# Kernel tuning notes

Measured on AMD Instinct MI355X. Metric: run time of the kernel, lower is better.

## Reference

```python
import jax, jax.numpy as jnp
import numpy as np

N_NODES = 100000
N_EDGES = 1600000
D = 64
NUM_HOPS = 3


def setup_inputs() -> dict:
    key = jax.random.key(0)
    ks = jax.random.split(key, 8)
    return {
        "H_l": jax.random.normal(ks[0], (N_NODES, D), dtype=jnp.float32),
        "edge_row": jax.random.randint(ks[1], (N_EDGES,), 0, N_NODES, dtype=jnp.int64),
        "edge_col": jax.random.randint(ks[2], (N_EDGES,), 0, N_NODES, dtype=jnp.int64),
        "edge_val": jax.random.uniform(ks[3], (N_EDGES,), dtype=jnp.float32),
        "out_degree": jax.random.uniform(ks[4], (N_NODES,), dtype=jnp.float32),
        "in_degree": jax.random.uniform(ks[5], (N_NODES,), dtype=jnp.float32),
        "hop_attention": jnp.ones((NUM_HOPS,), dtype=jnp.float32),
        "theta_out": jnp.full((NUM_HOPS,), 0.5, dtype=jnp.float32),
        "theta_in": jnp.full((NUM_HOPS,), 0.5, dtype=jnp.float32),
        "Theta": jax.random.normal(ks[6], (D, D), dtype=jnp.float32) * (6.0 ** 0.5) / (2 * D) ** 0.5,
    }


def reference(H_l, edge_row, edge_col, edge_val, out_degree, in_degree,
              hop_attention, theta_out, theta_in, Theta):
    n = H_l.shape[0]
    num_hops = hop_attention.shape[0]
    alpha = jax.nn.softmax(hop_attention)

    def spmm(rows, cols, X):
        # (A @ X)[r] = sum over edges (r,c): val * X[c]
        return jax.ops.segment_sum(edge_val[:, None] * X[cols], rows, num_segments=n)

    # fixed degree-scaled features (degrees clamped as in __init__)
    X_out = jnp.maximum(out_degree, 1e-8)[:, None] * H_l
    X_in = jnp.maximum(in_degree, 1e-8)[:, None] * H_l
    sum_term = jnp.zeros_like(H_l)
    for k in range(num_hops):
        # A^{k+1} @ (D_out H) computed by one more application of A per hop
        X_out = spmm(edge_row, edge_col, X_out)
        # (A^{k+1})^T @ (D_in H): transpose swaps row/col roles
        X_in = spmm(edge_col, edge_row, X_in)
        sum_term = sum_term + alpha[k] * (theta_out[k] * X_out + theta_in[k] * X_in)

    conv_term = jax.nn.sigmoid(sum_term @ Theta)
    return conv_term + H_l
```

## Files before the change

### kernel.cpp

```cpp
#include <hip/hip_runtime.h>
#include <hip/hip_fp16.h>

#define DFEAT 64
#define BKT_SHIFT 8
#define BKT_NODES 256
#define NBMAX 512
#define CH 4096
#define SRC_BITS 18
#define SRC_MASK ((1 << SRC_BITS) - 1)

__device__ __forceinline__ unsigned short f2h(float f) {
    return __half_as_ushort(__float2half(f));
}
__device__ __forceinline__ float h2f(unsigned short u) {
    return __half2float(__ushort_as_half(u));
}

__global__ void init_kernel(const float* __restrict__ H,
                            const float* __restrict__ outdeg,
                            const float* __restrict__ indeg,
                            const float* __restrict__ hop_att,
                            const float* __restrict__ th_out,
                            const float* __restrict__ th_in,
                            unsigned short* __restrict__ XAout,
                            unsigned short* __restrict__ XAin,
                            float* __restrict__ coefs, int n4) {
    int idx = blockIdx.x * blockDim.x + threadIdx.x;
    if (idx == 0) {
        float m = fmaxf(fmaxf(hop_att[0], hop_att[1]), hop_att[2]);
        float e0 = __expf(hop_att[0] - m);
        float e1 = __expf(hop_att[1] - m);
        float e2 = __expf(hop_att[2] - m);
        float inv = 1.0f / (e0 + e1 + e2);
        coefs[0] = e0 * inv * th_out[0]; coefs[1] = e0 * inv * th_in[0];
        coefs[2] = e1 * inv * th_out[1]; coefs[3] = e1 * inv * th_in[1];
        coefs[4] = e2 * inv * th_out[2]; coefs[5] = e2 * inv * th_in[2];
    }
    if (idx >= n4) return;
    int row = idx >> 4;
    float4 h = reinterpret_cast<const float4*>(H)[idx];
    float doo = fmaxf(outdeg[row], 1e-8f);
    float dii = fmaxf(indeg[row], 1e-8f);
    reinterpret_cast<ushort4*>(XAout)[idx] =
        make_ushort4(f2h(h.x * doo), f2h(h.y * doo), f2h(h.z * doo), f2h(h.w * doo));
    reinterpret_cast<ushort4*>(XAin)[idx] =
        make_ushort4(f2h(h.x * dii), f2h(h.y * dii), f2h(h.z * dii), f2h(h.w * dii));
}

__global__ __launch_bounds__(256) void hist2d_kernel(
        const int* __restrict__ erow, const int* __restrict__ ecol,
        int* __restrict__ cnt2, int nEdges, int nB, int nBlkA) {
    __shared__ int hR[NBMAX], hC[NBMAX];
    int k = blockIdx.x;
    for (int i = threadIdx.x; i < nB; i += 256) { hR[i] = 0; hC[i] = 0; }
    __syncthreads();
    int base = k * CH;
    int nV = min(CH, nEdges - base);
    for (int i = threadIdx.x; i < nV; i += 256) {
        atomicAdd(&hR[erow[base + i] >> BKT_SHIFT], 1);
        atomicAdd(&hC[ecol[base + i] >> BKT_SHIFT], 1);
    }
    __syncthreads();
    for (int b = threadIdx.x; b < nB; b += 256) {
        cnt2[(size_t)b * nBlkA + k] = hR[b];
        cnt2[((size_t)nB + b) * nBlkA + k] = hC[b];
    }
}

__global__ void scan_reduce1(const int* __restrict__ p, int* __restrict__ bsum,
                             int n) {
    int t = threadIdx.x, lane = t & 63, wid = t >> 6;
    int base = blockIdx.x * 1024 + t * 4;
    int s = 0;
#pragma unroll
    for (int i = 0; i < 4; ++i) { int idx = base + i; if (idx < n) s += p[idx]; }
#pragma unroll
    for (int o = 32; o >= 1; o >>= 1) s += __shfl_down(s, o, 64);
    __shared__ int wsum[4];
    if (lane == 0) wsum[wid] = s;
    __syncthreads();
    if (t == 0) bsum[blockIdx.x] = wsum[0] + wsum[1] + wsum[2] + wsum[3];
}

__global__ void scan_spine1(int* __restrict__ bsum, int nChunks) {
    int lane = threadIdx.x;
    int carry = 0;
    for (int base = 0; base < nChunks; base += 64) {
        int i = base + lane;
        int v = (i < nChunks) ? bsum[i] : 0;
        int s = v;
#pragma unroll
        for (int o = 1; o < 64; o <<= 1) {
            int x = __shfl_up(s, o, 64);
            if (lane >= o) s += x;
        }
        if (i < nChunks) bsum[i] = carry + s - v;
        carry += __shfl(s, 63, 64);
    }
}

__global__ void scan_down1(int* __restrict__ p, const int* __restrict__ bsum,
                           int n) {
    int t = threadIdx.x, lane = t & 63, wid = t >> 6;
    int base = blockIdx.x * 1024 + t * 4;
    int v[4];
    int tsum = 0;
#pragma unroll
    for (int i = 0; i < 4; ++i) {
        v[i] = (base + i < n) ? p[base + i] : 0;
        tsum += v[i];
    }
    int inc = tsum;
#pragma unroll
    for (int o = 1; o < 64; o <<= 1) {
        int x = __shfl_up(inc, o, 64);
        if (lane >= o) inc += x;
    }
    __shared__ int wsum[4];
    if (lane == 63) wsum[wid] = inc;
    __syncthreads();
    int woff = 0;
    for (int w = 0; w < wid; ++w) woff += wsum[w];
    int run = bsum[blockIdx.x] + woff + inc - tsum;
#pragma unroll
    for (int i = 0; i < 4; ++i) {
        if (base + i < n) p[base + i] = run;
        run += v[i];
    }
}

__global__ __launch_bounds__(256) void partA_kernel(
        const int* __restrict__ erow, const int* __restrict__ ecol,
        const float* __restrict__ eval, const int* __restrict__ base2,
        int2* __restrict__ recR, int2* __restrict__ recC,
        int nEdges, int nB, int nBlkA) {
    __shared__ int hist[NBMAX], scn[NBMAX], cur[NBMAX], gbase[NBMAX];
    __shared__ unsigned short keybuf[CH], slotKey[CH];
    __shared__ int2 stage[CH];
    int dir = blockIdx.y;
    const int* dk = dir ? ecol : erow;
    const int* ds = dir ? erow : ecol;
    int2* rec = dir ? recC : recR;
    int k = blockIdx.x;
    int base = k * CH;
    int nV = min(CH, nEdges - base);
    for (int i = threadIdx.x; i < nB; i += 256) {
        hist[i] = 0; cur[i] = 0;
        gbase[i] = base2[((size_t)dir * nB + i) * nBlkA + k] - dir * nEdges;
    }
    __syncthreads();
    for (int i = threadIdx.x; i < nV; i += 256) {
        int key = dk[base + i] >> BKT_SHIFT;
        keybuf[i] = (unsigned short)key;
        atomicAdd(&hist[key], 1);
    }
    __syncthreads();
    if (threadIdx.x < 64) {
        int lane = threadIdx.x;
        int carry = 0;
        for (int bb = 0; bb < nB; bb += 64) {
            int i = bb + lane;
            int v = (i < nB) ? hist[i] : 0;
            int s = v;
#pragma unroll
            for (int o = 1; o < 64; o <<= 1) {
                int x = __shfl_up(s, o, 64);
                if (lane >= o) s += x;
            }
            if (i < nB) scn[i] = carry + s - v;
            carry += __shfl(s, 63, 64);
        }
    }
    __syncthreads();
    for (int i = threadIdx.x; i < nV; i += 256) {
        int e = base + i;
        int key = keybuf[i];
        int slot = scn[key] + atomicAdd(&cur[key], 1);
        int dl = dk[e] & (BKT_NODES - 1);
        stage[slot] = make_int2(ds[e] | (dl << SRC_BITS), __float_as_int(eval[e]));
        slotKey[slot] = (unsigned short)key;
    }
    __syncthreads();
    for (int i = threadIdx.x; i < nV; i += 256) {
        int key = slotKey[i];
        rec[gbase[key] + (i - scn[key])] = stage[i];
    }
}

__global__ __launch_bounds__(256) void partB_kernel(
        const int2* __restrict__ recR, const int2* __restrict__ recC,
        const int* __restrict__ base2,
        int* __restrict__ rowptr, int* __restrict__ colptr,
        unsigned* __restrict__ pairsR, unsigned* __restrict__ pairsC,
        int nEdges, int nB, int nBlkA, int nNodes) {
    __shared__ int hist[BKT_NODES], scn[BKT_NODES], cur[BKT_NODES];
    int dir = blockIdx.y;
    int b = blockIdx.x;
    const int2* rec = dir ? recC : recR;
    unsigned* pairs = dir ? pairsC : pairsR;
    int* nptr = dir ? colptr : rowptr;
    int segB = base2[((size_t)dir * nB + b) * nBlkA] - dir * nEdges;
    int segE = (b == nB - 1) ? nEdges
             : base2[((size_t)dir * nB + b + 1) * nBlkA] - dir * nEdges;
    int t = threadIdx.x;
    hist[t] = 0; cur[t] = 0;
    __syncthreads();
    for (int j = segB + t; j < segE; j += 256)
        atomicAdd(&hist[(rec[j].x >> SRC_BITS) & (BKT_NODES - 1)], 1);
    __syncthreads();
    if (t < 64) {
        int lane = t, carry = 0;
        for (int bb = 0; bb < BKT_NODES; bb += 64) {
            int i = bb + lane;
            int v = hist[i], s = v;
#pragma unroll
            for (int o = 1; o < 64; o <<= 1) {
                int x = __shfl_up(s, o, 64);
                if (lane >= o) s += x;
            }
            scn[i] = carry + s - v;
            carry += __shfl(s, 63, 64);
        }
    }
    __syncthreads();
    int node = (b << BKT_SHIFT) + t;
    if (node < nNodes) nptr[node] = segB + scn[t];
    if (b == nB - 1 && t == 0) nptr[nNodes] = nEdges;
    for (int j = segB + t; j < segE; j += 256) {
        int2 r = rec[j];
        int dl = (r.x >> SRC_BITS) & (BKT_NODES - 1);
        int slot = segB + scn[dl] + atomicAdd(&cur[dl], 1);
        unsigned vh = f2h(__int_as_float(r.y)) & 0x7FFFu;
        pairs[slot] = ((unsigned)(r.x & SRC_MASK) << 15) | vh;
    }
}

template <int FIRST, int LAST>
__global__ __launch_bounds__(256) void spmm_split(
        const int* __restrict__ rowptr, const unsigned* __restrict__ pairsR,
        const int* __restrict__ colptr, const unsigned* __restrict__ pairsC,
        const __half* __restrict__ Xout, const __half* __restrict__ Xin,
        unsigned short* __restrict__ Yout, unsigned short* __restrict__ Yin,
        unsigned short* __restrict__ sumO, unsigned short* __restrict__ sumI,
        const float* __restrict__ coefs, int k, int nNodes) {
    int b = blockIdx.x;
    int slot = b & 7;
    int dir = slot >> 2;
    int g = (b >> 3) * 4 + (slot & 3);
    int wid = threadIdx.x >> 6;
    int lane = threadIdx.x & 63;
    int node = g * 4 + wid;
    if (node >= nNodes) return;

    const int* ptr = dir ? colptr : rowptr;
    const unsigned* pairs = dir ? pairsC : pairsR;
    const __half* X = dir ? Xin : Xout;
    unsigned short* Y = dir ? Yin : Yout;
    unsigned short* sm = dir ? sumI : sumO;
    float cf = coefs[2 * k + dir];

    int hb = lane >> 5;
    int sub = lane & 31;

    float2 a0 = {0.f, 0.f}, a1 = {0.f, 0.f}, a2 = {0.f, 0.f}, a3 = {0.f, 0.f};
    int bE = ptr[node], eE = ptr[node + 1];
    int j = bE;
    for (; j + 8 <= eE; j += 8) {
        unsigned p0 = pairs[j     + hb];
        unsigned p1 = pairs[j + 2 + hb];
        unsigned p2 = pairs[j + 4 + hb];
        unsigned p3 = pairs[j + 6 + hb];
        float2 x0 = __half22float2(*(const __half2*)(X + (p0 >> 15) * DFEAT + 2 * sub));
        float2 x1 = __half22float2(*(const __half2*)(X + (p1 >> 15) * DFEAT + 2 * sub));
        float2 x2 = __half22float2(*(const __half2*)(X + (p2 >> 15) * DFEAT + 2 * sub));
        float2 x3 = __half22float2(*(const __half2*)(X + (p3 >> 15) * DFEAT + 2 * sub));
        float v0 = h2f(p0 & 0x7FFFu);
        float v1 = h2f(p1 & 0x7FFFu);
        float v2 = h2f(p2 & 0x7FFFu);
        float v3 = h2f(p3 & 0x7FFFu);
        a0.x += v0 * x0.x; a0.y += v0 * x0.y;
        a1.x += v1 * x1.x; a1.y += v1 * x1.y;
        a2.x += v2 * x2.x; a2.y += v2 * x2.y;
        a3.x += v3 * x3.x; a3.y += v3 * x3.y;
    }
    if (j < eE) {
#pragma unroll
        for (int q = 0; q < 4; ++q) {
            int idx = j + 2 * q + hb;
            unsigned p = (idx < eE) ? pairs[idx] : 0u;
            float2 x = __half22float2(*(const __half2*)(X + (p >> 15) * DFEAT + 2 * sub));
            float v = h2f(p & 0x7FFFu);
            a0.x += v * x.x; a0.y += v * x.y;
        }
    }
    float ax = (a0.x + a1.x) + (a2.x + a3.x);
    float ay = (a0.y + a1.y) + (a2.y + a3.y);
    ax += __shfl_xor(ax, 32, 64);
    ay += __shfl_xor(ay, 32, 64);

    if (hb == 0) {
        int off = node * DFEAT + 2 * sub;
        if (!LAST) {
            __half2 yv = __floats2half2_rn(ax, ay);
            __builtin_nontemporal_store(*reinterpret_cast<unsigned*>(&yv),
                                        reinterpret_cast<unsigned*>(Y + off));
        }
        float sx = cf * ax, sy = cf * ay;
        if (!FIRST) {
            __half2 old = *reinterpret_cast<const __half2*>(sm + off);
            float2 of = __half22float2(old);
            sx += of.x; sy += of.y;
        }
        __half2 sv = __floats2half2_rn(sx, sy);
        __builtin_nontemporal_store(*reinterpret_cast<unsigned*>(&sv),
                                    reinterpret_cast<unsigned*>(sm + off));
    }
}

__global__ __launch_bounds__(256) void final_kernel(
        const unsigned short* __restrict__ sumO,
        const unsigned short* __restrict__ sumI,
        const float* __restrict__ H, const float* __restrict__ Theta,
        float* __restrict__ out, int nRows) {
    __shared__ float Th[64 * 64];
    __shared__ float Srow[4 * 64];
    int t = threadIdx.x;
    for (int i = t; i < 64 * 64; i += 256) Th[i] = Theta[i];
    int rl = t >> 6;
    int c = t & 63;
    int row = blockIdx.x * 4 + rl;
    int off = row * DFEAT + c;
    float sv = (row < nRows) ? h2f(sumO[off]) + h2f(sumI[off]) : 0.f;
    Srow[rl * 64 + c] = sv;
    __syncthreads();
    if (row >= nRows) return;
    float acc = 0.f;
#pragma unroll
    for (int kk = 0; kk < 64; ++kk) acc += Srow[rl * 64 + kk] * Th[kk * 64 + c];
    float r = 1.0f / (1.0f + __expf(-acc)) + H[off];
    __builtin_nontemporal_store(r, &out[off]);
}

extern "C" void kernel_launch(void* const* d_in, const int* in_sizes, int n_in,
                              void* d_out, int out_size, void* d_ws, size_t ws_size,
                              hipStream_t stream) {
    const float* H      = (const float*)d_in[0];
    const int*   erow   = (const int*)d_in[1];
    const int*   ecol   = (const int*)d_in[2];
    const float* eval   = (const float*)d_in[3];
    const float* outdeg = (const float*)d_in[4];
    const float* indeg  = (const float*)d_in[5];
    const float* hopatt = (const float*)d_in[6];
    const float* thout  = (const float*)d_in[7];
    const float* thin   = (const float*)d_in[8];
    const float* Theta  = (const float*)d_in[9];
    float* out = (float*)d_out;

    int nNodes = in_sizes[0] / DFEAT;
    int nEdges = in_sizes[1];

    char* ws = (char*)d_ws;
    size_t off = 0;
    auto alloc = [&](size_t bytes) {
        void* p = ws + off;
        off += (bytes + 255) & ~(size_t)255;
        return p;
    };
    size_t xBytes = (size_t)nNodes * DFEAT * sizeof(unsigned short);
    unsigned short* XAout = (unsigned short*)alloc(xBytes);
    unsigned short* XAin  = (unsigned short*)alloc(xBytes);
    unsigned short* XBout = (unsigned short*)alloc(xBytes);
    unsigned short* XBin  = (unsigned short*)alloc(xBytes);
    unsigned short* sumO  = (unsigned short*)alloc(xBytes);
    unsigned short* sumI  = (unsigned short*)alloc(xBytes);
    int*   rowptr = (int*)alloc((size_t)(nNodes + 1) * sizeof(int));
    int*   colptr = (int*)alloc((size_t)(nNodes + 1) * sizeof(int));
    int2*  recR   = (int2*)alloc((size_t)nEdges * sizeof(int2));
    int2*  recC   = (int2*)alloc((size_t)nEdges * sizeof(int2));
    unsigned* pairsR = (unsigned*)alloc((size_t)nEdges * sizeof(unsigned));
    unsigned* pairsC = (unsigned*)alloc((size_t)nEdges * sizeof(unsigned));

    int nB    = (nNodes + BKT_NODES - 1) >> BKT_SHIFT;
    int nBlkA = (nEdges + CH - 1) / CH;
    int L = 2 * nB * nBlkA;
    int nChunks = (L + 1023) / 1024;
    int*   cnt2 = (int*)alloc((size_t)L * sizeof(int));
    int*   bsum = (int*)alloc((size_t)nChunks * sizeof(int));
    float* coefs = (float*)alloc(8 * sizeof(float));

    int n4 = nNodes * (DFEAT / 4);
    int ewBlocks = (n4 + 255) / 256;
    int gPerDir = (nNodes + 3) / 4;
    int grid8 = (gPerDir + 3) / 4;
    int splitGrid = 8 * grid8;

    init_kernel<<<ewBlocks, 256, 0, stream>>>(H, outdeg, indeg, hopatt, thout, thin,
                                              XAout, XAin, coefs, n4);
    hist2d_kernel<<<nBlkA, 256, 0, stream>>>(erow, ecol, cnt2, nEdges, nB, nBlkA);
    scan_reduce1<<<nChunks, 256, 0, stream>>>(cnt2, bsum, L);
    scan_spine1<<<1, 64, 0, stream>>>(bsum, nChunks);
    scan_down1<<<nChunks, 256, 0, stream>>>(cnt2, bsum, L);
    partA_kernel<<<dim3(nBlkA, 2), 256, 0, stream>>>(erow, ecol, eval, cnt2,
                                                     recR, recC, nEdges, nB, nBlkA);
    partB_kernel<<<dim3(nB, 2), 256, 0, stream>>>(recR, recC, cnt2,
                                                  rowptr, colptr, pairsR, pairsC,
                                                  nEdges, nB, nBlkA, nNodes);

    spmm_split<1, 0><<<splitGrid, 256, 0, stream>>>(rowptr, pairsR, colptr, pairsC,
                                                    (const __half*)XAout, (const __half*)XAin,
                                                    XBout, XBin, sumO, sumI,
                                                    coefs, 0, nNodes);
    spmm_split<0, 0><<<splitGrid, 256, 0, stream>>>(rowptr, pairsR, colptr, pairsC,
                                                    (const __half*)XBout, (const __half*)XBin,
                                                    XAout, XAin, sumO, sumI,
                                                    coefs, 1, nNodes);
    spmm_split<0, 1><<<splitGrid, 256, 0, stream>>>(rowptr, pairsR, colptr, pairsC,
                                                    (const __half*)XAout, (const __half*)XAin,
                                                    nullptr, nullptr, sumO, sumI,
                                                    coefs, 2, nNodes);

    final_kernel<<<(nNodes + 3) / 4, 256, 0, stream>>>(sumO, sumI, H, Theta,
                                                       out, nNodes);
}
```

Baseline: 462.8 us.

## Fuse last-hop SpMM with final Theta projection and deepen gather unroll

Merges the third hop's SpMM for both directions into the final projection kernel. Each wave gathers its node's out and in aggregates, adds them to the running sums, and applies Theta plus sigmoid directly, so the last sumO/sumI write and reread and one launch go away. The gather loop is also unrolled to 16 edges with 8 accumulators for more memory-level parallelism. The cost is that the fused kernel does both directions per wave, which halves parallelism for that hop and raises register pressure.

After: 412.1 us. -10.9%, faster.

```diff
diff --git a/kernel.cpp b/kernel.cpp
--- a/kernel.cpp
+++ b/kernel.cpp
@@ -235,7 +235,43 @@
     }
 }
 
-template <int FIRST, int LAST>
+__device__ __forceinline__ void gather_rows(
+        const int* __restrict__ ptr, const unsigned* __restrict__ pairs,
+        const __half* __restrict__ X, int node, int hb, int sub,
+        float& axo, float& ayo) {
+    float2 a0{0.f,0.f}, a1{0.f,0.f}, a2{0.f,0.f}, a3{0.f,0.f};
+    float2 a4{0.f,0.f}, a5{0.f,0.f}, a6{0.f,0.f}, a7{0.f,0.f};
+    int j = ptr[node], eE = ptr[node + 1];
+    auto step = [&](int jj, float2& a) {
+        unsigned p = pairs[jj + hb];
+        float2 x = __half22float2(*(const __half2*)(X + (p >> 15) * DFEAT + 2 * sub));
+        float v = h2f(p & 0x7FFFu);
+        a.x += v * x.x; a.y += v * x.y;
+    };
+    for (; j + 16 <= eE; j += 16) {
+        step(j, a0);      step(j + 2, a1);  step(j + 4, a2);  step(j + 6, a3);
+        step(j + 8, a4);  step(j + 10, a5); step(j + 12, a6); step(j + 14, a7);
+    }
+    if (j + 8 <= eE) {
+        step(j, a0); step(j + 2, a1); step(j + 4, a2); step(j + 6, a3);
+        j += 8;
+    }
+#pragma unroll
+    for (int q = 0; q < 4; ++q) {
+        int idx = j + 2 * q + hb;
+        unsigned p = (idx < eE) ? pairs[idx] : 0u;
+        float2 x = __half22float2(*(const __half2*)(X + (p >> 15) * DFEAT + 2 * sub));
+        float v = h2f(p & 0x7FFFu);
+        a4.x += v * x.x; a4.y += v * x.y;
+    }
+    float ax = ((a0.x + a1.x) + (a2.x + a3.x)) + ((a4.x + a5.x) + (a6.x + a7.x));
+    float ay = ((a0.y + a1.y) + (a2.y + a3.y)) + ((a4.y + a5.y) + (a6.y + a7.y));
+    ax += __shfl_xor(ax, 32, 64);
+    ay += __shfl_xor(ay, 32, 64);
+    axo = ax; ayo = ay;
+}
+
+template <int FIRST>
 __global__ __launch_bounds__(256) void spmm_split(
         const int* __restrict__ rowptr, const unsigned* __restrict__ pairsR,
         const int* __restrict__ colptr, const unsigned* __restrict__ pairsC,
@@ -262,49 +298,14 @@
     int hb = lane >> 5;
     int sub = lane & 31;
 
-    float2 a0 = {0.f, 0.f}, a1 = {0.f, 0.f}, a2 = {0.f, 0.f}, a3 = {0.f, 0.f};
-    int bE = ptr[node], eE = ptr[node + 1];
-    int j = bE;
-    for (; j + 8 <= eE; j += 8) {
-        unsigned p0 = pairs[j     + hb];
-        unsigned p1 = pairs[j + 2 + hb];
-        unsigned p2 = pairs[j + 4 + hb];
-        unsigned p3 = pairs[j + 6 + hb];
-        float2 x0 = __half22float2(*(const __half2*)(X + (p0 >> 15) * DFEAT + 2 * sub));
-        float2 x1 = __half22float2(*(const __half2*)(X + (p1 >> 15) * DFEAT + 2 * sub));
-        float2 x2 = __half22float2(*(const __half2*)(X + (p2 >> 15) * DFEAT + 2 * sub));
-        float2 x3 = __half22float2(*(const __half2*)(X + (p3 >> 15) * DFEAT + 2 * sub));
-        float v0 = h2f(p0 & 0x7FFFu);
-        float v1 = h2f(p1 & 0x7FFFu);
-        float v2 = h2f(p2 & 0x7FFFu);
-        float v3 = h2f(p3 & 0x7FFFu);
-        a0.x += v0 * x0.x; a0.y += v0 * x0.y;
-        a1.x += v1 * x1.x; a1.y += v1 * x1.y;
-        a2.x += v2 * x2.x; a2.y += v2 * x2.y;
-        a3.x += v3 * x3.x; a3.y += v3 * x3.y;
-    }
-    if (j < eE) {
-#pragma unroll
-        for (int q = 0; q < 4; ++q) {
-            int idx = j + 2 * q + hb;
-            unsigned p = (idx < eE) ? pairs[idx] : 0u;
-            float2 x = __half22float2(*(const __half2*)(X + (p >> 15) * DFEAT + 2 * sub));
-            float v = h2f(p & 0x7FFFu);
-            a0.x += v * x.x; a0.y += v * x.y;
-        }
-    }
-    float ax = (a0.x + a1.x) + (a2.x + a3.x);
-    float ay = (a0.y + a1.y) + (a2.y + a3.y);
-    ax += __shfl_xor(ax, 32, 64);
-    ay += __shfl_xor(ay, 32, 64);
+    float ax, ay;
+    gather_rows(ptr, pairs, X, node, hb, sub, ax, ay);
 
     if (hb == 0) {
         int off = node * DFEAT + 2 * sub;
-        if (!LAST) {
-            __half2 yv = __floats2half2_rn(ax, ay);
-            __builtin_nontemporal_store(*reinterpret_cast<unsigned*>(&yv),
-                                        reinterpret_cast<unsigned*>(Y + off));
-        }
+        __half2 yv = __floats2half2_rn(ax, ay);
+        __builtin_nontemporal_store(*reinterpret_cast<unsigned*>(&yv),
+                                    reinterpret_cast<unsigned*>(Y + off));
         float sx = cf * ax, sy = cf * ay;
         if (!FIRST) {
             __half2 old = *reinterpret_cast<const __half2*>(sm + off);
@@ -317,28 +318,50 @@
     }
 }
 
-__global__ __launch_bounds__(256) void final_kernel(
+__global__ __launch_bounds__(256) void spmm_last(
+        const int* __restrict__ rowptr, const unsigned* __restrict__ pairsR,
+        const int* __restrict__ colptr, const unsigned* __restrict__ pairsC,
+        const __half* __restrict__ Xout, const __half* __restrict__ Xin,
         const unsigned short* __restrict__ sumO,
         const unsigned short* __restrict__ sumI,
         const float* __restrict__ H, const float* __restrict__ Theta,
-        float* __restrict__ out, int nRows) {
+        float* __restrict__ out, const float* __restrict__ coefs,
+        int k, int nNodes) {
     __shared__ float Th[64 * 64];
     __shared__ float Srow[4 * 64];
-    int t = threadIdx.x;
-    for (int i = t; i < 64 * 64; i += 256) Th[i] = Theta[i];
-    int rl = t >> 6;
-    int c = t & 63;
-    int row = blockIdx.x * 4 + rl;
-    int off = row * DFEAT + c;
-    float sv = (row < nRows) ? h2f(sumO[off]) + h2f(sumI[off]) : 0.f;
-    Srow[rl * 64 + c] = sv;
-    __syncthreads();
-    if (row >= nRows) return;
+    int wid = threadIdx.x >> 6;
+    int lane = threadIdx.x & 63;
+    int node = blockIdx.x * 4 + wid;
+    bool live = node < nNodes;
+    int nodeC = live ? node : 0;
+
+    for (int i = threadIdx.x; i < 64 * 64; i += 256) Th[i] = Theta[i];
+
+    float co = coefs[2 * k], ci = coefs[2 * k + 1];
+    int hb = lane >> 5;
+    int sub = lane & 31;
+
+    float axO, ayO, axI, ayI;
+    gather_rows(rowptr, pairsR, Xout, nodeC, hb, sub, axO, ayO);
+    gather_rows(colptr, pairsC, Xin,  nodeC, hb, sub, axI, ayI);
+
+    int off = nodeC * DFEAT + 2 * sub;
+    float s0 = h2f(sumO[off])     + h2f(sumI[off])     + co * axO + ci * axI;
+    float s1 = h2f(sumO[off + 1]) + h2f(sumI[off + 1]) + co * ayO + ci * ayI;
+
+    __syncthreads();
+    if (hb == 0) {
+        Srow[wid * 64 + 2 * sub]     = s0;
+        Srow[wid * 64 + 2 * sub + 1] = s1;
+    }
     float acc = 0.f;
 #pragma unroll
-    for (int kk = 0; kk < 64; ++kk) acc += Srow[rl * 64 + kk] * Th[kk * 64 + c];
-    float r = 1.0f / (1.0f + __expf(-acc)) + H[off];
-    __builtin_nontemporal_store(r, &out[off]);
+    for (int kk = 0; kk < 64; ++kk)
+        acc += Srow[wid * 64 + kk] * Th[kk * 64 + lane];
+    if (live) {
+        float r = 1.0f / (1.0f + __expf(-acc)) + H[nodeC * DFEAT + lane];
+        __builtin_nontemporal_store(r, &out[nodeC * DFEAT + lane]);
+    }
 }
 
 extern "C" void kernel_launch(void* const* d_in, const int* in_sizes, int n_in,
@@ -393,6 +416,7 @@
     int gPerDir = (nNodes + 3) / 4;
     int grid8 = (gPerDir + 3) / 4;
     int splitGrid = 8 * grid8;
+    int nodeBlocks = (nNodes + 3) / 4;
 
     init_kernel<<<ewBlocks, 256, 0, stream>>>(H, outdeg, indeg, hopatt, thout, thin,
                                               XAout, XAin, coefs, n4);
@@ -406,19 +430,17 @@
                                                   rowptr, colptr, pairsR, pairsC,
                                                   nEdges, nB, nBlkA, nNodes);
 
-    spmm_split<1, 0><<<splitGrid, 256, 0, stream>>>(rowptr, pairsR, colptr, pairsC,
-                                                    (const __half*)XAout, (const __half*)XAin,
-                                                    XBout, XBin, sumO, sumI,
-                                                    coefs, 0, nNodes);
-    spmm_split<0, 0><<<splitGrid, 256, 0, stream>>>(rowptr, pairsR, colptr, pairsC,
-                                                    (const __half*)XBout, (const __half*)XBin,
-                                                    XAout, XAin, sumO, sumI,
-                                                    coefs, 1, nNodes);
-    spmm_split<0, 1><<<splitGrid, 256, 0, stream>>>(rowptr, pairsR, colptr, pairsC,
-                                                    (const __half*)XAout, (const __half*)XAin,
-                                                    nullptr, nullptr, sumO, sumI,
-                                                    coefs, 2, nNodes);
-
-    final_kernel<<<(nNodes + 3) / 4, 256, 0, stream>>>(sumO, sumI, H, Theta,
-                                                       out, nNodes);
-}
+    spmm_split<1><<<splitGrid, 256, 0, stream>>>(rowptr, pairsR, colptr, pairsC,
+                                                 (const __half*)XAout, (const __half*)XAin,
+                                                 XBout, XBin, sumO, sumI,
+                                                 coefs, 0, nNodes);
+    spmm_split<0><<<splitGrid, 256, 0, stream>>>(rowptr, pairsR, colptr, pairsC,
+                                                 (const __half*)XBout, (const __half*)XBin,
+                                                 XAout, XAin, sumO, sumI,
+                                                 coefs, 1, nNodes);
+
+    spmm_last<<<nodeBlocks, 256, 0, stream>>>(rowptr, pairsR, colptr, pairsC,
+                                              (const __half*)XAout, (const __half*)XAin,
+                                              sumO, sumI, H, Theta, out,
+                                              coefs, 2, nNodes);
+}
```
